# Performance work log

Measured on AMD Instinct MI355X. Metric: run time of the kernel, lower is better.

Reference implementation:

```python
import jax, jax.numpy as jnp
import numpy as np

B, C, H, W = 8, 256, 64, 64
D = C // 8  # query/key channels


def setup_inputs() -> dict:
    key = jax.random.key(0)
    ks = jax.random.split(key, 7)
    s = 0.05
    x = jax.random.normal(ks[0], (B, C, H, W), dtype=jnp.float32)
    Wq = jax.random.normal(ks[1], (D, C), dtype=jnp.float32) * s
    bq = jax.random.normal(ks[2], (D,), dtype=jnp.float32) * s
    Wk = jax.random.normal(ks[3], (D, C), dtype=jnp.float32) * s
    bk = jax.random.normal(ks[4], (D,), dtype=jnp.float32) * s
    Wv = jax.random.normal(ks[5], (C, C), dtype=jnp.float32) * s
    bv = jax.random.normal(ks[6], (C,), dtype=jnp.float32) * s
    return {"x": x, "Wq": Wq, "bq": bq, "Wk": Wk, "bk": bk, "Wv": Wv, "bv": bv}


def reference(x, Wq, bq, Wk, bk, Wv, bv):
    b, c, h, w = x.shape
    n = h * w
    xf = x.reshape(b, c, n)  # (B, C, HW)
    # 1x1 convs == per-pixel linear projections
    q = jnp.einsum('dc,bcn->bdn', Wq, xf) + bq[None, :, None]  # (B, D, HW)
    k = jnp.einsum('dc,bcn->bdn', Wk, xf) + bk[None, :, None]  # (B, D, HW)
    v = jnp.einsum('ec,bcn->ben', Wv, xf) + bv[None, :, None]  # (B, C, HW)
    # attention[b, n, m] = sum_d q[b,d,n] * k[b,d,m]  (no 1/sqrt(d) scaling)
    attn = jax.nn.softmax(jnp.einsum('bdn,bdm->bnm', q, k), axis=-1)
    # out[b,c,n] = sum_m v[b,c,m] * attn[b,n,m]  (v @ attn^T)
    out = jnp.einsum('bcm,bnm->bcn', v, attn)
    return out.reshape(b, c, h, w) + x
```

## Files before the change

### kernel.cpp

```cpp
#include <hip/hip_runtime.h>
#include <stdint.h>

#define BN 4096
#define NCH 256
#define DQ 32

typedef _Float16 half8  __attribute__((ext_vector_type(8)));
typedef _Float16 half4  __attribute__((ext_vector_type(4)));
typedef _Float16 half2  __attribute__((ext_vector_type(2)));
typedef float   floatx4  __attribute__((ext_vector_type(4)));
typedef float   floatx16 __attribute__((ext_vector_type(16)));

typedef __attribute__((address_space(1))) const void g1_void;
typedef __attribute__((address_space(3))) void l3_void;

#define LOG2E 1.44269504088896f
#define EXP2F(x) __builtin_amdgcn_exp2f(x)
#define LOG2F(x) __builtin_amdgcn_logf(x)

__global__ __launch_bounds__(256) void convert_w(
    const float* __restrict__ Wq, const float* __restrict__ Wk,
    const float* __restrict__ Wv, _Float16* __restrict__ W16)
{
    int e4 = (blockIdx.x * 256 + threadIdx.x) * 4;
    float4 v;
    if (e4 < 8192)        v = *(const float4*)&Wq[e4];
    else if (e4 < 16384) {
        v = *(const float4*)&Wk[e4 - 8192];
        v.x *= LOG2E; v.y *= LOG2E; v.z *= LOG2E; v.w *= LOG2E;
    }
    else                  v = *(const float4*)&Wv[e4 - 16384];
    half4 h = { (_Float16)v.x, (_Float16)v.y, (_Float16)v.z, (_Float16)v.w };
    *(half4*)&W16[e4] = h;
}

__global__ __launch_bounds__(512) void proj_kernel(
    const float* __restrict__ x, const _Float16* __restrict__ W16,
    const float* __restrict__ bq, const float* __restrict__ bk,
    const float* __restrict__ bv,
    _Float16* __restrict__ qT, _Float16* __restrict__ kT,
    _Float16* __restrict__ vb)
{
    const int t  = threadIdx.x;
    const int n0 = blockIdx.x * 128;
    const int b  = blockIdx.y;

    __shared__ __align__(16) _Float16 xTl[128 * 256];

#pragma unroll
    for (int p = 0; p < 2; ++p) {
        const int kb = p * 128 + (t >> 5) * 8;
        const int n4 = (t & 31) * 4;
        float4 xr[8];
#pragma unroll
        for (int i = 0; i < 8; ++i)
            xr[i] = *(const float4*)&x[((size_t)b * NCH + kb + i) * BN + n0 + n4];
        const float* xf = (const float*)xr;
#pragma unroll
        for (int j = 0; j < 4; ++j) {
            const int n = n4 + j;
            half8 hv;
#pragma unroll
            for (int i = 0; i < 8; ++i) hv[i] = (_Float16)xf[i * 4 + j];
            const int phys = (kb >> 3) ^ ((n >> 2) & 31);
            *(half8*)&xTl[n * 256 + phys * 8] = hv;
        }
    }
    __syncthreads();

    const int lane  = t & 63;
    const int w     = t >> 6;
    const int col32 = lane & 31;
    const int h     = lane >> 5;
    const int nc    = w & 3;
    const int job   = w >> 2;

    const _Float16* Wq16 = W16;
    const _Float16* Wk16 = W16 + 8192;
    const _Float16* Wv16 = W16 + 16384;

#define XFRAG(ks) (*(const half8*)&xTl[(nc * 32 + col32) * 256 + \
        (((ks) * 2 + h) ^ (((nc * 32 + col32) >> 2) & 31)) * 8])

    if (job == 0) {
        const float bqv = bq[col32];
        const float bkv = bk[col32] * LOG2E;
        floatx16 aq, ak2;
#pragma unroll
        for (int r = 0; r < 16; ++r) { aq[r] = 0.0f; ak2[r] = 0.0f; }
#pragma unroll
        for (int ks = 0; ks < 16; ++ks) {
            half8 xa = XFRAG(ks);
            half8 wqf = *(const half8*)&Wq16[col32 * 256 + ks * 16 + h * 8];
            half8 wkf = *(const half8*)&Wk16[col32 * 256 + ks * 16 + h * 8];
            aq  = __builtin_amdgcn_mfma_f32_32x32x16_f16(xa, wqf, aq, 0, 0, 0);
            ak2 = __builtin_amdgcn_mfma_f32_32x32x16_f16(xa, wkf, ak2, 0, 0, 0);
        }
#pragma unroll
        for (int r = 0; r < 16; ++r) {
            const int n = n0 + nc * 32 + (r & 3) + 8 * (r >> 2) + 4 * h;
            qT[((size_t)b * BN + n) * DQ + col32] = (_Float16)(aq[r] + bqv);
            kT[((size_t)b * BN + n) * DQ + col32] = (_Float16)(ak2[r] + bkv);
        }
    }

    const int rg_lo = (job == 0) ? 0 : 3;
    const int rg_hi = (job == 0) ? 3 : 8;
    for (int rg = rg_lo; rg < rg_hi; ++rg) {
        floatx16 av;
#pragma unroll
        for (int r = 0; r < 16; ++r) av[r] = 0.0f;
#pragma unroll
        for (int ks = 0; ks < 16; ++ks) {
            half8 xb  = XFRAG(ks);
            half8 wvf = *(const half8*)&Wv16[(rg * 32 + col32) * 256 + ks * 16 + h * 8];
            av = __builtin_amdgcn_mfma_f32_32x32x16_f16(wvf, xb, av, 0, 0, 0);
        }
#pragma unroll
        for (int r = 0; r < 16; ++r) {
            const int c = rg * 32 + (r & 3) + 8 * (r >> 2) + 4 * h;
            vb[((size_t)b * NCH + c) * BN + n0 + nc * 32 + col32] =
                (_Float16)(av[r] + bv[c]);
        }
    }
#undef XFRAG
}

__global__ __launch_bounds__(256, 3) void flash_kernel(
    const _Float16* __restrict__ qT, const _Float16* __restrict__ kT,
    const _Float16* __restrict__ vb,
    _Float16* __restrict__ Op, float* __restrict__ Ml, int KPS)
{
    const int t    = threadIdx.x;
    const int lane = t & 63;
    const int w    = t >> 6;
    const int n0   = blockIdx.x * 64;
    const int kh   = blockIdx.y;
    const int b    = blockIdx.z;
    const int kbase = kh * KPS;
    const int iters = (min(KPS, BN - kbase)) >> 6;

    __shared__ __align__(16) _Float16 vs[NCH * 64];
    __shared__ __align__(16) _Float16 Ps[2][64 * 64];
    __shared__ float alph_s[2][64];
    __shared__ float l_s[64];

    const int col   = lane & 15;
    const int q4    = lane >> 4;
    const int col32 = lane & 31;
    const int h     = lane >> 5;

    const _Float16* kp = kT + (size_t)b * BN * DQ;
    const _Float16* vp = vb + (size_t)b * NCH * BN;

    half8 bqf = *(const half8*)&qT[((size_t)b * BN + n0 + w * 16 + col) * DQ + q4 * 8];

    floatx16 acc[2][2];
#pragma unroll
    for (int ct = 0; ct < 2; ++ct)
#pragma unroll
        for (int nt = 0; nt < 2; ++nt)
#pragma unroll
            for (int r = 0; r < 16; ++r) acc[ct][nt][r] = 0.0f;

    float m_i = -1e30f, l_i = 0.0f;

    const int sc_loc = lane >> 3;
    const int s_log  = (lane & 7) ^ (sc_loc & 7);

    half8 ak[4];
    floatx4 sf[4];
    half4 pk[4];
    float al;

#define K_LOAD(MC)                                                          \
    do {                                                                    \
        _Pragma("unroll")                                                   \
        for (int mt = 0; mt < 4; ++mt)                                      \
            ak[mt] = *(const half8*)&kp[(size_t)((MC) + mt * 16 + col) * DQ + q4 * 8]; \
    } while (0)

#define V_DMA(MC)                                                           \
    do {                                                                    \
        _Pragma("unroll")                                                   \
        for (int j = 0; j < 8; ++j) {                                       \
            const int c = w * 64 + j * 8 + sc_loc;                          \
            __builtin_amdgcn_global_load_lds(                               \
                (g1_void*)&vp[(size_t)c * BN + (MC) + s_log * 8],           \
                (l3_void*)&vs[(w * 64 + j * 8) * 64], 16, 0, 0);            \
        }                                                                   \
    } while (0)

#define QK_STEP()                                                           \
    do {                                                                    \
        __builtin_amdgcn_s_setprio(1);                                      \
        _Pragma("unroll")                                                   \
        for (int mt = 0; mt < 4; ++mt) {                                    \
            floatx4 z = { 0.0f, 0.0f, 0.0f, 0.0f };                         \
            sf[mt] = __builtin_amdgcn_mfma_f32_16x16x32_f16(ak[mt], bqf, z, 0, 0, 0); \
        }                                                                   \
        __builtin_amdgcn_s_setprio(0);                                      \
    } while (0)

#define SM_STEP()                                                           \
    do {                                                                    \
        float cmax = -1e30f;                                                \
        _Pragma("unroll")                                                   \
        for (int mt = 0; mt < 4; ++mt)                                      \
            _Pragma("unroll")                                               \
            for (int r = 0; r < 4; ++r) cmax = fmaxf(cmax, sf[mt][r]);      \
        cmax = fmaxf(cmax, __shfl_xor(cmax, 16));                           \
        cmax = fmaxf(cmax, __shfl_xor(cmax, 32));                           \
        const float mn = (cmax > m_i + 8.0f) ? cmax : m_i;                  \
        al = EXP2F(m_i - mn);                                               \
        float csum = 0.0f;                                                  \
        _Pragma("unroll")                                                   \
        for (int mt = 0; mt < 4; ++mt) {                                    \
            float p0 = EXP2F(sf[mt][0] - mn);                               \
            float p1 = EXP2F(sf[mt][1] - mn);                               \
            float p2 = EXP2F(sf[mt][2] - mn);                               \
            float p3 = EXP2F(sf[mt][3] - mn);                               \
            csum += p0 + p1 + p2 + p3;                                      \
            half2 q01 = __builtin_bit_cast(half2, __builtin_amdgcn_cvt_pkrtz(p0, p1)); \
            half2 q23 = __builtin_bit_cast(half2, __builtin_amdgcn_cvt_pkrtz(p2, p3)); \
            pk[mt][0] = q01[0]; pk[mt][1] = q01[1];                         \
            pk[mt][2] = q23[0]; pk[mt][3] = q23[1];                         \
        }                                                                   \
        csum += __shfl_xor(csum, 16);                                       \
        csum += __shfl_xor(csum, 32);                                       \
        l_i = l_i * al + csum;                                              \
        m_i = mn;                                                           \
    } while (0)

#define PS_WRITE(BUF)                                                       \
    do {                                                                    \
        const int n = w * 16 + col;                                         \
        _Pragma("unroll")                                                   \
        for (int mt = 0; mt < 4; ++mt) {                                    \
            const int p_log = 2 * mt + (q4 >> 1);                           \
            const int p_phys = p_log ^ (n & 7);                             \
            *(half4*)((char*)&Ps[BUF][n * 64] + p_phys * 16 + (q4 & 1) * 8) = pk[mt]; \
        }                                                                   \
        if (q4 == 0) alph_s[BUF][n] = al;                                   \
    } while (0)

#define RESCALE(BUF)                                                        \
    do {                                                                    \
        float a0 = alph_s[BUF][col32];                                      \
        float a1 = alph_s[BUF][32 + col32];                                 \
        if (!__all((a0 == 1.0f) && (a1 == 1.0f))) {                         \
            _Pragma("unroll")                                               \
            for (int ct = 0; ct < 2; ++ct)                                  \
                _Pragma("unroll")                                           \
                for (int r = 0; r < 16; ++r) {                              \
                    acc[ct][0][r] *= a0;                                    \
                    acc[ct][1][r] *= a1;                                    \
                }                                                           \
        }                                                                   \
    } while (0)

#define PV_STEP(BUF)                                                        \
    do {                                                                    \
        __builtin_amdgcn_s_setprio(1);                                      \
        _Pragma("unroll")                                                   \
        for (int ks = 0; ks < 4; ++ks) {                                    \
            const int p_log = 2 * ks + h;                                   \
            half8 bp0 = *(const half8*)((char*)&Ps[BUF][col32 * 64] + (p_log ^ (col32 & 7)) * 16); \
            half8 bp1 = *(const half8*)((char*)&Ps[BUF][(32 + col32) * 64] + (p_log ^ (col32 & 7)) * 16); \
            _Pragma("unroll")                                               \
            for (int ct = 0; ct < 2; ++ct) {                                \
                const int c = w * 64 + ct * 32 + col32;                     \
                half8 av = *(const half8*)((char*)&vs[c * 64] + ((p_log ^ (c & 7)) * 16)); \
                acc[ct][0] = __builtin_amdgcn_mfma_f32_32x32x16_f16(av, bp0, acc[ct][0], 0, 0, 0); \
                acc[ct][1] = __builtin_amdgcn_mfma_f32_32x32x16_f16(av, bp1, acc[ct][1], 0, 0, 0); \
            }                                                               \
        }                                                                   \
        __builtin_amdgcn_s_setprio(0);                                      \
    } while (0)

    K_LOAD(kbase);
    V_DMA(kbase);
    QK_STEP();
    { const int m1 = (1 < iters) ? kbase + 64 : kbase; K_LOAD(m1); }
    SM_STEP();
    PS_WRITE(0);

    for (int it = 0; it < iters - 1; ++it) {
        const int cur = it & 1, nxt = cur ^ 1;
        asm volatile("s_waitcnt lgkmcnt(0)" ::: "memory");
        __builtin_amdgcn_s_barrier();
        QK_STEP();
        { const int m2 = (it + 2 < iters) ? kbase + (it + 2) * 64
                                          : kbase + (iters - 1) * 64;
          K_LOAD(m2); }
        RESCALE(cur);
        asm volatile("s_waitcnt vmcnt(4)" ::: "memory");
        PV_STEP(cur);
        SM_STEP();
        PS_WRITE(nxt);
        asm volatile("s_waitcnt lgkmcnt(0)" ::: "memory");
        V_DMA(kbase + (it + 1) * 64);
    }

    {
        const int cur = (iters - 1) & 1;
        asm volatile("s_waitcnt lgkmcnt(0)" ::: "memory");
        __builtin_amdgcn_s_barrier();
        RESCALE(cur);
        asm volatile("s_waitcnt vmcnt(0)" ::: "memory");
        PV_STEP(cur);
    }

    if (q4 == 0) {
        const int n = w * 16 + col;
        l_s[n] = l_i;
        Ml[(size_t)(kh * 8 + b) * BN + n0 + n] = m_i + LOG2F(l_i);
    }
    __syncthreads();
    const float li0 = 1.0f / l_s[col32];
    const float li1 = 1.0f / l_s[32 + col32];

    _Float16* Opp = Op + (size_t)(kh * 8 + b) * NCH * BN;
#pragma unroll
    for (int ct = 0; ct < 2; ++ct)
#pragma unroll
        for (int nt = 0; nt < 2; ++nt) {
            const float li = nt ? li1 : li0;
#pragma unroll
            for (int r = 0; r < 16; ++r) {
                int row = (r & 3) + 8 * (r >> 2) + 4 * h;
                int c = w * 64 + ct * 32 + row;
                Opp[(size_t)c * BN + n0 + nt * 32 + col32] = (_Float16)(acc[ct][nt][r] * li);
            }
        }
#undef K_LOAD
#undef V_DMA
#undef QK_STEP
#undef SM_STEP
#undef PS_WRITE
#undef RESCALE
#undef PV_STEP
}

__global__ __launch_bounds__(256) void combine_kernel(
    const _Float16* __restrict__ Op, const float* __restrict__ Ml,
    const float* __restrict__ x, float* __restrict__ out, int nsplit)
{
    const int n  = (blockIdx.x * 256 + threadIdx.x) * 8;
    const int c0 = blockIdx.y * 2;
    const int b  = blockIdx.z;

    float f[3][8];
    float Z[8];
#pragma unroll
    for (int j = 0; j < 8; ++j) Z[j] = -1e30f;
    for (int s = 0; s < nsplit; ++s) {
        const float* mlp = &Ml[(size_t)(s * 8 + b) * BN + n];
        floatx4 z0 = *(const floatx4*)mlp;
        floatx4 z1 = *(const floatx4*)(mlp + 4);
#pragma unroll
        for (int j = 0; j < 4; ++j) { f[s][j] = z0[j]; f[s][4 + j] = z1[j]; }
#pragma unroll
        for (int j = 0; j < 8; ++j) Z[j] = fmaxf(Z[j], f[s][j]);
    }
    float lsum[8];
#pragma unroll
    for (int j = 0; j < 8; ++j) lsum[j] = 0.0f;
    for (int s = 0; s < nsplit; ++s)
#pragma unroll
        for (int j = 0; j < 8; ++j) { f[s][j] = EXP2F(f[s][j] - Z[j]); lsum[j] += f[s][j]; }
#pragma unroll
    for (int j = 0; j < 8; ++j) lsum[j] = 1.0f / lsum[j];
    for (int s = 0; s < nsplit; ++s)
#pragma unroll
        for (int j = 0; j < 8; ++j) f[s][j] *= lsum[j];

#pragma unroll 2
    for (int ci = 0; ci < 2; ++ci) {
        const int c = c0 + ci;
        const size_t off = ((size_t)b * NCH + c) * BN + n;
        const size_t po = (size_t)c * BN + n;
        float ov[8];
#pragma unroll
        for (int j = 0; j < 8; ++j) ov[j] = 0.0f;
        for (int s = 0; s < nsplit; ++s) {
            half8 hv = *(const half8*)&Op[(size_t)(s * 8 + b) * NCH * BN + po];
#pragma unroll
            for (int j = 0; j < 8; ++j) ov[j] += (float)hv[j] * f[s][j];
        }
        floatx4 x0 = *(const floatx4*)&x[off];
        floatx4 x1 = *(const floatx4*)&x[off + 4];
        floatx4 o0, o1;
#pragma unroll
        for (int j = 0; j < 4; ++j) { o0[j] = ov[j] + x0[j]; o1[j] = ov[4 + j] + x1[j]; }
        *(floatx4*)&out[off] = o0;
        *(floatx4*)&out[off + 4] = o1;
    }
}

extern "C" void kernel_launch(void* const* d_in, const int* in_sizes, int n_in,
                              void* d_out, int out_size, void* d_ws, size_t ws_size,
                              hipStream_t stream)
{
    const float* x  = (const float*)d_in[0];
    const float* Wq = (const float*)d_in[1];
    const float* bq = (const float*)d_in[2];
    const float* Wk = (const float*)d_in[3];
    const float* bk = (const float*)d_in[4];
    const float* Wv = (const float*)d_in[5];
    const float* bv = (const float*)d_in[6];
    float* out = (float*)d_out;

    _Float16* ws = (_Float16*)d_ws;
    _Float16* W16 = ws;
    _Float16* qT  = W16 + 81920;
    _Float16* kT  = qT + (size_t)8 * BN * DQ;
    _Float16* vb  = kT + (size_t)8 * BN * DQ;
    _Float16* Op  = vb + (size_t)8 * NCH * BN;

    const size_t baseElems = 81920 + (size_t)2 * 8 * BN * DQ + (size_t)8 * NCH * BN;
    const size_t opElems3  = (size_t)3 * 8 * NCH * BN;
    const size_t mlBytes   = (size_t)24 * BN * sizeof(float);
    const size_t need3     = (baseElems + opElems3) * 2 + mlBytes + 256;
    const int nsplit = (ws_size >= need3) ? 3 : 2;
    const int KPS    = (nsplit == 3) ? 1408 : 2048;

    float* Ml = (float*)(Op + (size_t)nsplit * 8 * NCH * BN);

    convert_w<<<dim3(80), 256, 0, stream>>>(Wq, Wk, Wv, W16);
    proj_kernel<<<dim3(32, 8), 512, 0, stream>>>(x, W16, bq, bk, bv, qT, kT, vb);
    flash_kernel<<<dim3(64, nsplit, 8), 256, 0, stream>>>(qT, kT, vb, Op, Ml, KPS);
    combine_kernel<<<dim3(2, 128, 8), 256, 0, stream>>>(Op, Ml, x, out, nsplit);
}
```

Before: 237.5 us.

## Warp-specialize flash kernel into QK/softmax producer and PV consumer waves

```diff
diff --git a/kernel.cpp b/kernel.cpp
--- a/kernel.cpp
+++ b/kernel.cpp
@@ -126,14 +126,16 @@
 #undef XFRAG
 }
 
-__global__ __launch_bounds__(256, 3) void flash_kernel(
+__global__ __launch_bounds__(512, 4) void flash_kernel(
     const _Float16* __restrict__ qT, const _Float16* __restrict__ kT,
     const _Float16* __restrict__ vb,
     _Float16* __restrict__ Op, float* __restrict__ Ml, int KPS)
 {
     const int t    = threadIdx.x;
     const int lane = t & 63;
-    const int w    = t >> 6;
+    const int wid  = t >> 6;
+    const int w    = wid & 3;
+    const bool is_prod = (wid < 4);
     const int n0   = blockIdx.x * 64;
     const int kh   = blockIdx.y;
     const int b    = blockIdx.z;
@@ -153,25 +155,16 @@
     const _Float16* kp = kT + (size_t)b * BN * DQ;
     const _Float16* vp = vb + (size_t)b * NCH * BN;
 
-    half8 bqf = *(const half8*)&qT[((size_t)b * BN + n0 + w * 16 + col) * DQ + q4 * 8];
-
+    half8 bqf{};
+    half8 ak[4];
+    float m_i = -1e30f, l_i = 0.0f;
+    float al = 0.0f;
+    floatx4 sf[4];
+    half4 pk[4];
     floatx16 acc[2][2];
-#pragma unroll
-    for (int ct = 0; ct < 2; ++ct)
-#pragma unroll
-        for (int nt = 0; nt < 2; ++nt)
-#pragma unroll
-            for (int r = 0; r < 16; ++r) acc[ct][nt][r] = 0.0f;
-
-    float m_i = -1e30f, l_i = 0.0f;
 
     const int sc_loc = lane >> 3;
     const int s_log  = (lane & 7) ^ (sc_loc & 7);
-
-    half8 ak[4];
-    floatx4 sf[4];
-    half4 pk[4];
-    float al;
 
 #define K_LOAD(MC)                                                          \
     do {                                                                    \
@@ -193,13 +186,11 @@
 
 #define QK_STEP()                                                           \
     do {                                                                    \
-        __builtin_amdgcn_s_setprio(1);                                      \
         _Pragma("unroll")                                                   \
         for (int mt = 0; mt < 4; ++mt) {                                    \
             floatx4 z = { 0.0f, 0.0f, 0.0f, 0.0f };                         \
             sf[mt] = __builtin_amdgcn_mfma_f32_16x16x32_f16(ak[mt], bqf, z, 0, 0, 0); \
         }                                                                   \
-        __builtin_amdgcn_s_setprio(0);                                      \
     } while (0)
 
 #define SM_STEP()                                                           \
@@ -278,61 +269,71 @@
         __builtin_amdgcn_s_setprio(0);                                      \
     } while (0)
 
-    K_LOAD(kbase);
-    V_DMA(kbase);
-    QK_STEP();
-    { const int m1 = (1 < iters) ? kbase + 64 : kbase; K_LOAD(m1); }
-    SM_STEP();
-    PS_WRITE(0);
-
-    for (int it = 0; it < iters - 1; ++it) {
+    if (is_prod) {
+        bqf = *(const half8*)&qT[((size_t)b * BN + n0 + w * 16 + col) * DQ + q4 * 8];
+        K_LOAD(kbase);
+        QK_STEP();
+        { const int m1 = (1 < iters) ? kbase + 64 : kbase; K_LOAD(m1); }
+        SM_STEP();
+        PS_WRITE(0);
+    } else {
+#pragma unroll
+        for (int ct = 0; ct < 2; ++ct)
+#pragma unroll
+            for (int nt = 0; nt < 2; ++nt)
+#pragma unroll
+                for (int r = 0; r < 16; ++r) acc[ct][nt][r] = 0.0f;
+        V_DMA(kbase);
+    }
+
+    for (int it = 0; it < iters; ++it) {
         const int cur = it & 1, nxt = cur ^ 1;
         asm volatile("s_waitcnt lgkmcnt(0)" ::: "memory");
         __builtin_amdgcn_s_barrier();
-        QK_STEP();
-        { const int m2 = (it + 2 < iters) ? kbase + (it + 2) * 64
-                                          : kbase + (iters - 1) * 64;
-          K_LOAD(m2); }
-        RESCALE(cur);
-        asm volatile("s_waitcnt vmcnt(4)" ::: "memory");
-        PV_STEP(cur);
-        SM_STEP();
-        PS_WRITE(nxt);
-        asm volatile("s_waitcnt lgkmcnt(0)" ::: "memory");
-        V_DMA(kbase + (it + 1) * 64);
-    }
-
-    {
-        const int cur = (iters - 1) & 1;
-        asm volatile("s_waitcnt lgkmcnt(0)" ::: "memory");
-        __builtin_amdgcn_s_barrier();
-        RESCALE(cur);
-        asm volatile("s_waitcnt vmcnt(0)" ::: "memory");
-        PV_STEP(cur);
-    }
-
-    if (q4 == 0) {
+
+        if (is_prod) {
+            if (it + 1 < iters) {
+                QK_STEP();
+                { const int m2 = (it + 2 < iters) ? kbase + (it + 2) * 64
+                                                  : kbase + (iters - 1) * 64;
+                  K_LOAD(m2); }
+                SM_STEP();
+                PS_WRITE(nxt);
+            }
+        } else {
+            RESCALE(cur);
+            asm volatile("s_waitcnt vmcnt(0)" ::: "memory");
+            PV_STEP(cur);
+            if (it + 1 < iters) {
+                asm volatile("s_waitcnt lgkmcnt(0)" ::: "memory");
+                V_DMA(kbase + (it + 1) * 64);
+            }
+        }
+    }
+
+    if (is_prod && q4 == 0) {
         const int n = w * 16 + col;
         l_s[n] = l_i;
         Ml[(size_t)(kh * 8 + b) * BN + n0 + n] = m_i + LOG2F(l_i);
     }
     __syncthreads();
-    const float li0 = 1.0f / l_s[col32];
-    const float li1 = 1.0f / l_s[32 + col32];
-
-    _Float16* Opp = Op + (size_t)(kh * 8 + b) * NCH * BN;
-#pragma unroll
-    for (int ct = 0; ct < 2; ++ct)
-#pragma unroll
-        for (int nt = 0; nt < 2; ++nt) {
-            const float li = nt ? li1 : li0;
-#pragma unroll
-            for (int r = 0; r < 16; ++r) {
-                int row = (r & 3) + 8 * (r >> 2) + 4 * h;
-                int c = w * 64 + ct * 32 + row;
-                Opp[(size_t)c * BN + n0 + nt * 32 + col32] = (_Float16)(acc[ct][nt][r] * li);
+    if (!is_prod) {
+        const float li0 = 1.0f / l_s[col32];
+        const float li1 = 1.0f / l_s[32 + col32];
+        _Float16* Opp = Op + (size_t)(kh * 8 + b) * NCH * BN;
+#pragma unroll
+        for (int ct = 0; ct < 2; ++ct)
+#pragma unroll
+            for (int nt = 0; nt < 2; ++nt) {
+                const float li = nt ? li1 : li0;
+#pragma unroll
+                for (int r = 0; r < 16; ++r) {
+                    int row = (r & 3) + 8 * (r >> 2) + 4 * h;
+                    int c = w * 64 + ct * 32 + row;
+                    Opp[(size_t)c * BN + n0 + nt * 32 + col32] = (_Float16)(acc[ct][nt][r] * li);
+                }
             }
-        }
+    }
 #undef K_LOAD
 #undef V_DMA
 #undef QK_STEP
@@ -429,6 +430,6 @@
 
     convert_w<<<dim3(80), 256, 0, stream>>>(Wq, Wk, Wv, W16);
     proj_kernel<<<dim3(32, 8), 512, 0, stream>>>(x, W16, bq, bk, bv, qT, kT, vb);
-    flash_kernel<<<dim3(64, nsplit, 8), 256, 0, stream>>>(qT, kT, vb, Op, Ml, KPS);
+    flash_kernel<<<dim3(64, nsplit, 8), 512, 0, stream>>>(qT, kT, vb, Op, Ml, KPS);
     combine_kernel<<<dim3(2, 128, 8), 256, 0, stream>>>(Op, Ml, x, out, nsplit);
 }
```

After: 378.4 us. 1.59x slower.
